# Performance work log

Hardware: AMD Instinct MI355X
Metric: run time of the kernel (lower is better)

Reference implementation:

```python
import jax, jax.numpy as jnp
import numpy as np

N = 8192
IN_F = 256
OUT_F = 128


def setup_inputs() -> dict:
    key = jax.random.key(0)
    k1, k2, k3, k4, k5, k6 = jax.random.split(key, 6)
    input = jax.random.normal(k1, (N, IN_F), dtype=jnp.float32)
    adj = jax.random.randint(k2, (N, N), 0, 2, dtype=jnp.int32)
    # xavier-uniform-like init scaled by gain=0.5
    def xavier(k, shape, gain=0.5):
        fan_in, fan_out = shape[0], shape[1]
        lim = gain * np.sqrt(6.0 / (fan_in + fan_out))
        return jax.random.uniform(k, shape, dtype=jnp.float32, minval=-lim, maxval=lim)
    W_s = xavier(k3, (IN_F, OUT_F))
    a_s = xavier(k4, (OUT_F, 1))
    W_n = xavier(k5, (IN_F, OUT_F))
    a_n = xavier(k6, (OUT_F, 1))
    return {"input": input, "adj": adj, "W_s": W_s, "a_s": a_s, "W_n": W_n, "a_n": a_n}


def reference(input, adj, W_s, a_s, W_n, a_n):
    # Projections: [N, out_features]
    h_s = input @ W_s
    h_n = input @ W_n
    # Additive attention logits: e[i, j] = relu((h_s @ a_s)[i] + (h_n @ a_n)[j])
    e = jax.nn.relu((h_s @ a_s) + (h_n @ a_n).T)  # [N, N]
    # Masked softmax over neighbors (dim=1)
    attention = jnp.where(adj > 0, e, jnp.float32(-9e15))
    attention = jax.nn.softmax(attention, axis=1)
    # Self-scaling term (sum of softmax rows, kept for faithfulness)
    attention_sum = jnp.sum(attention, axis=-1, keepdims=True)
    attention_s = 1.0 / (1.0 + attention_sum)
    # Dropout is identity in eval mode (p=0 / training=False)
    h_prime = attention_s * h_s + attention @ h_n
    # concat=True -> elu activation
    return jax.nn.elu(h_prime)
```

## Files before the change

### kernel.cpp

```cpp
#include <hip/hip_runtime.h>
#include <math.h>

#define NN 8192

typedef short short8 __attribute__((ext_vector_type(8)));
typedef float f32x4 __attribute__((ext_vector_type(4)));

__device__ __forceinline__ float eluf(float x) {
  return x > 0.f ? x : (__expf(x) - 1.f);
}
__device__ __forceinline__ unsigned short f2bf(float f) {
  union { float f; unsigned u; } v; v.f = f;
  unsigned r = v.u + 0x7fffu + ((v.u >> 16) & 1u);
  return (unsigned short)(r >> 16);
}

__global__ __launch_bounds__(256) void k_proj(const float* __restrict__ X,
                                              const float* __restrict__ Ws,
                                              const float* __restrict__ Wn,
                                              const float* __restrict__ as_,
                                              const float* __restrict__ an_,
                                              float* __restrict__ Hs,
                                              unsigned short* __restrict__ HnT,
                                              float* __restrict__ s_out,
                                              float* __restrict__ n_out) {
  __shared__ float4 lin4[8 * 64];
  const int t = threadIdx.x;
  const int i0 = blockIdx.x * 8;
  const float4* Xg = (const float4*)X + (size_t)i0 * 64;
  lin4[t] = Xg[t];
  if (t < 256) lin4[t + 256] = Xg[t + 256];
  __syncthreads();
  const int c = t & 127;
  const int rh = t >> 7;
  float accs[4], accn[4];
#pragma unroll
  for (int r = 0; r < 4; ++r) { accs[r] = 0.f; accn[r] = 0.f; }
  for (int k = 0; k < 256; k += 4) {
    float ws0 = Ws[(k + 0) * 128 + c], ws1 = Ws[(k + 1) * 128 + c];
    float ws2 = Ws[(k + 2) * 128 + c], ws3 = Ws[(k + 3) * 128 + c];
    float wn0 = Wn[(k + 0) * 128 + c], wn1 = Wn[(k + 1) * 128 + c];
    float wn2 = Wn[(k + 2) * 128 + c], wn3 = Wn[(k + 3) * 128 + c];
#pragma unroll
    for (int r = 0; r < 4; ++r) {
      float4 iv = lin4[(rh * 4 + r) * 64 + (k >> 2)];
      accs[r] = fmaf(iv.x, ws0, accs[r]); accs[r] = fmaf(iv.y, ws1, accs[r]);
      accs[r] = fmaf(iv.z, ws2, accs[r]); accs[r] = fmaf(iv.w, ws3, accs[r]);
      accn[r] = fmaf(iv.x, wn0, accn[r]); accn[r] = fmaf(iv.y, wn1, accn[r]);
      accn[r] = fmaf(iv.z, wn2, accn[r]); accn[r] = fmaf(iv.w, wn3, accn[r]);
    }
  }
#pragma unroll
  for (int r = 0; r < 4; ++r)
    Hs[(size_t)(i0 + rh * 4 + r) * 128 + c] = accs[r];
  {
    union { unsigned short us[4]; ushort4 u4; } pk;
#pragma unroll
    for (int r = 0; r < 4; ++r) pk.us[r] = f2bf(accn[r]);
    *(ushort4*)(HnT + (size_t)blockIdx.x * 1024 + c * 8 + rh * 4) = pk.u4;
  }
  float* red = (float*)lin4;
  const int wv = t >> 6, ln = t & 63;
  __syncthreads();
  {
    float av = as_[c];
#pragma unroll
    for (int r = 0; r < 4; ++r) red[(rh * 4 + r) * 128 + c] = accs[r] * av;
  }
  __syncthreads();
#pragma unroll
  for (int h = 0; h < 2; ++h) {
    int row = wv * 2 + h;
    float p = red[row * 128 + ln] + red[row * 128 + 64 + ln];
#pragma unroll
    for (int off = 32; off >= 1; off >>= 1) p += __shfl_down(p, off);
    if (ln == 0) s_out[i0 + row] = p;
  }
  __syncthreads();
  {
    float av = an_[c];
#pragma unroll
    for (int r = 0; r < 4; ++r) red[(rh * 4 + r) * 128 + c] = accn[r] * av;
  }
  __syncthreads();
#pragma unroll
  for (int h = 0; h < 2; ++h) {
    int row = wv * 2 + h;
    float p = red[row * 128 + ln] + red[row * 128 + 64 + ln];
#pragma unroll
    for (int off = 32; off >= 1; off >>= 1) p += __shfl_down(p, off);
    if (ln == 0) n_out[i0 + row] = p;
  }
}

__global__ __launch_bounds__(512, 4) void k_main(const int* __restrict__ A,
                                                 const unsigned short* __restrict__ HnT,
                                                 const float* __restrict__ sv_g,
                                                 const float* __restrict__ nv_g,
                                                 float* __restrict__ HsOut) {
  __shared__ float accbuf[8][16][128];
  __shared__ float zsh[8][16];
  __shared__ float zf[16];

  const int t = threadIdx.x;
  const int wv = t >> 6;
  const int ln = t & 63;
  const int q = ln >> 4;
  const int m = ln & 15;
  const int row0 = blockIdx.x * 16;

  const float sm = sv_g[row0 + m];
  const int jbase = wv * 1024 + q * 8;
  const int* aptr = A + (size_t)(row0 + m) * NN + jbase;
  const float* nptr = nv_g + jbase;
  const unsigned short* bptr = HnT + ((size_t)(wv * 128 + q) * 128 + m) * 8;

  f32x4 acc[8];
#pragma unroll
  for (int ft = 0; ft < 8; ++ft) acc[ft] = (f32x4){0.f, 0.f, 0.f, 0.f};
  float zp = 0.f;

  int4 adjv[2][2];
  float4 nvv[2][2];
  union Breg { uint4 u; short8 s; };
  Breg breg[8];

  adjv[0][0] = *(const int4*)(aptr);       adjv[0][1] = *(const int4*)(aptr + 4);
  adjv[1][0] = *(const int4*)(aptr + 32);  adjv[1][1] = *(const int4*)(aptr + 36);
  nvv[0][0] = *(const float4*)(nptr);      nvv[0][1] = *(const float4*)(nptr + 4);
  breg[0].u = *(const uint4*)(bptr);       breg[1].u = *(const uint4*)(bptr + 128);
  breg[2].u = *(const uint4*)(bptr + 256); breg[3].u = *(const uint4*)(bptr + 384);
  breg[4].u = *(const uint4*)(bptr + 512); breg[5].u = *(const uint4*)(bptr + 640);
  breg[6].u = *(const uint4*)(bptr + 768); breg[7].u = *(const uint4*)(bptr + 896);

#pragma unroll 2
  for (int tt = 0; tt < 32; ++tt) {
    const int cur = tt & 1;
    short8 fr;
    {
      float nvl[8] = {nvv[cur][0].x, nvv[cur][0].y, nvv[cur][0].z, nvv[cur][0].w,
                      nvv[cur][1].x, nvv[cur][1].y, nvv[cur][1].z, nvv[cur][1].w};
      int av[8] = {adjv[cur][0].x, adjv[cur][0].y, adjv[cur][0].z, adjv[cur][0].w,
                   adjv[cur][1].x, adjv[cur][1].y, adjv[cur][1].z, adjv[cur][1].w};
#pragma unroll
      for (int k = 0; k < 8; ++k) {
        float w = av[k] > 0 ? __expf(fmaxf(sm + nvl[k], 0.f)) : 0.f;
        zp += w;
        fr[k] = (short)f2bf(w);
      }
    }
    if (tt < 31) {
      const float* p = nptr + (tt + 1) * 32;
      nvv[cur ^ 1][0] = *(const float4*)p;
      nvv[cur ^ 1][1] = *(const float4*)(p + 4);
    }
    __builtin_amdgcn_s_setprio(1);
    acc[0] = __builtin_amdgcn_mfma_f32_16x16x32_bf16(fr, breg[0].s, acc[0], 0, 0, 0);
    acc[1] = __builtin_amdgcn_mfma_f32_16x16x32_bf16(fr, breg[1].s, acc[1], 0, 0, 0);
    acc[2] = __builtin_amdgcn_mfma_f32_16x16x32_bf16(fr, breg[2].s, acc[2], 0, 0, 0);
    acc[3] = __builtin_amdgcn_mfma_f32_16x16x32_bf16(fr, breg[3].s, acc[3], 0, 0, 0);
    acc[4] = __builtin_amdgcn_mfma_f32_16x16x32_bf16(fr, breg[4].s, acc[4], 0, 0, 0);
    acc[5] = __builtin_amdgcn_mfma_f32_16x16x32_bf16(fr, breg[5].s, acc[5], 0, 0, 0);
    acc[6] = __builtin_amdgcn_mfma_f32_16x16x32_bf16(fr, breg[6].s, acc[6], 0, 0, 0);
    acc[7] = __builtin_amdgcn_mfma_f32_16x16x32_bf16(fr, breg[7].s, acc[7], 0, 0, 0);
    __builtin_amdgcn_s_setprio(0);
    if (tt < 31) {
      const unsigned short* p = bptr + (size_t)(tt + 1) * 4096;
      breg[0].u = *(const uint4*)(p);       breg[1].u = *(const uint4*)(p + 128);
      breg[2].u = *(const uint4*)(p + 256); breg[3].u = *(const uint4*)(p + 384);
      breg[4].u = *(const uint4*)(p + 512); breg[5].u = *(const uint4*)(p + 640);
      breg[6].u = *(const uint4*)(p + 768); breg[7].u = *(const uint4*)(p + 896);
    }
    if (tt < 30) {
      const int* p = aptr + (tt + 2) * 32;
      adjv[cur][0] = *(const int4*)p;
      adjv[cur][1] = *(const int4*)(p + 4);
    }
  }

  {
    float zz = zp;
    zz += __shfl_down(zz, 32);
    zz += __shfl_down(zz, 16);
    if (ln < 16) zsh[wv][ln] = zz;
  }
#pragma unroll
  for (int ft = 0; ft < 8; ++ft) {
#pragma unroll
    for (int reg = 0; reg < 4; ++reg)
      accbuf[wv][q * 4 + reg][ft * 16 + m] = acc[ft][reg];
  }
  __syncthreads();
  if (t < 16) {
    float z = zsh[0][t] + zsh[1][t] + zsh[2][t] + zsh[3][t] +
              zsh[4][t] + zsh[5][t] + zsh[6][t] + zsh[7][t];
    zf[t] = 1.f / z;
  }
  __syncthreads();
  {
    const int row = t >> 5;
    const int f0 = (t & 31) * 4;
    f32x4 ssum = *(const f32x4*)&accbuf[0][row][f0];
#pragma unroll
    for (int w = 1; w < 8; ++w) ssum += *(const f32x4*)&accbuf[w][row][f0];
    const float invz = zf[row];
    const size_t off = (size_t)(row0 + row) * 128 + f0;
    float4 h = *(const float4*)(HsOut + off);
    float4 o;
    o.x = eluf(fmaf(ssum[0], invz, 0.5f * h.x));
    o.y = eluf(fmaf(ssum[1], invz, 0.5f * h.y));
    o.z = eluf(fmaf(ssum[2], invz, 0.5f * h.z));
    o.w = eluf(fmaf(ssum[3], invz, 0.5f * h.w));
    *(float4*)(HsOut + off) = o;
  }
}

extern "C" void kernel_launch(void* const* d_in, const int* in_sizes, int n_in,
                              void* d_out, int out_size, void* d_ws, size_t ws_size,
                              hipStream_t stream) {
  const float* X   = (const float*)d_in[0];
  const int*   A   = (const int*)d_in[1];
  const float* Ws  = (const float*)d_in[2];
  const float* as_ = (const float*)d_in[3];
  const float* Wn  = (const float*)d_in[4];
  const float* an_ = (const float*)d_in[5];
  float* out = (float*)d_out;

  unsigned short* HnT = (unsigned short*)d_ws;
  float* s = (float*)(HnT + (size_t)128 * NN);
  float* n = s + NN;

  k_proj<<<1024, 256, 0, stream>>>(X, Ws, Wn, as_, an_, out, HnT, s, n);
  k_main<<<512, 512, 0, stream>>>(A, HnT, s, n, out);
}
```

Measured before the change: 459.7 us.

## Pack int32 adjacency into bitmask before the attention aggregation kernel

Adds a pre-pass kernel that compresses each row of the int32 adjacency matrix into 32-bit bitmasks, so the main kernel reads 1 bit per neighbour instead of 4 bytes. The main kernel now prefetches one mask word and extracts a byte per lane group instead of loading int4 vectors. The full adjacency read still happens, now in a separate pass with no compute overlapping it, plus an extra write and read of the packed mask. The packing keeps only the low bit, which matches `adj > 0` only for 0/1 values. The original path is kept as a fallback when the workspace is too small.

New measurement: 451.9 us. Within noise of the previous version (-1.7%).

```diff
diff --git a/kernel.cpp b/kernel.cpp
--- a/kernel.cpp
+++ b/kernel.cpp
@@ -13,6 +13,25 @@
   union { float f; unsigned u; } v; v.f = f;
   unsigned r = v.u + 0x7fffu + ((v.u >> 16) & 1u);
   return (unsigned short)(r >> 16);
+}
+
+__global__ __launch_bounds__(256) void k_pack(const int* __restrict__ A,
+                                              unsigned* __restrict__ P) {
+  const int t = threadIdx.x;
+  const int row = blockIdx.x;
+  const int4* src = (const int4*)(A + (size_t)row * NN) + t * 8;
+  int4 v[8];
+#pragma unroll
+  for (int c = 0; c < 8; ++c) v[c] = src[c];
+  unsigned w = 0;
+#pragma unroll
+  for (int c = 0; c < 8; ++c) {
+    w |= (unsigned)(v[c].x & 1) << (c * 4 + 0);
+    w |= (unsigned)(v[c].y & 1) << (c * 4 + 1);
+    w |= (unsigned)(v[c].z & 1) << (c * 4 + 2);
+    w |= (unsigned)(v[c].w & 1) << (c * 4 + 3);
+  }
+  P[(size_t)row * 256 + t] = w;
 }
 
 __global__ __launch_bounds__(256) void k_proj(const float* __restrict__ X,
@@ -93,11 +112,11 @@
   }
 }
 
-__global__ __launch_bounds__(512, 4) void k_main(const int* __restrict__ A,
-                                                 const unsigned short* __restrict__ HnT,
-                                                 const float* __restrict__ sv_g,
-                                                 const float* __restrict__ nv_g,
-                                                 float* __restrict__ HsOut) {
+__global__ __launch_bounds__(512, 4) void k_main_bits(const unsigned* __restrict__ Pk,
+                                                      const unsigned short* __restrict__ HnT,
+                                                      const float* __restrict__ sv_g,
+                                                      const float* __restrict__ nv_g,
+                                                      float* __restrict__ HsOut) {
   __shared__ float accbuf[8][16][128];
   __shared__ float zsh[8][16];
   __shared__ float zf[16];
@@ -111,8 +130,8 @@
 
   const float sm = sv_g[row0 + m];
   const int jbase = wv * 1024 + q * 8;
-  const int* aptr = A + (size_t)(row0 + m) * NN + jbase;
   const float* nptr = nv_g + jbase;
+  const unsigned* Pp = Pk + (size_t)(row0 + m) * 256 + wv * 32;
   const unsigned short* bptr = HnT + ((size_t)(wv * 128 + q) * 128 + m) * 8;
 
   f32x4 acc[8];
@@ -120,14 +139,15 @@
   for (int ft = 0; ft < 8; ++ft) acc[ft] = (f32x4){0.f, 0.f, 0.f, 0.f};
   float zp = 0.f;
 
-  int4 adjv[2][2];
   float4 nvv[2][2];
+  unsigned bv[2];
   union Breg { uint4 u; short8 s; };
   Breg breg[8];
 
-  adjv[0][0] = *(const int4*)(aptr);       adjv[0][1] = *(const int4*)(aptr + 4);
-  adjv[1][0] = *(const int4*)(aptr + 32);  adjv[1][1] = *(const int4*)(aptr + 36);
   nvv[0][0] = *(const float4*)(nptr);      nvv[0][1] = *(const float4*)(nptr + 4);
+  nvv[1][0] = *(const float4*)(nptr + 32); nvv[1][1] = *(const float4*)(nptr + 36);
+  bv[0] = Pp[0];
+  bv[1] = Pp[1];
   breg[0].u = *(const uint4*)(bptr);       breg[1].u = *(const uint4*)(bptr + 128);
   breg[2].u = *(const uint4*)(bptr + 256); breg[3].u = *(const uint4*)(bptr + 384);
   breg[4].u = *(const uint4*)(bptr + 512); breg[5].u = *(const uint4*)(bptr + 640);
@@ -140,19 +160,19 @@
     {
       float nvl[8] = {nvv[cur][0].x, nvv[cur][0].y, nvv[cur][0].z, nvv[cur][0].w,
                       nvv[cur][1].x, nvv[cur][1].y, nvv[cur][1].z, nvv[cur][1].w};
-      int av[8] = {adjv[cur][0].x, adjv[cur][0].y, adjv[cur][0].z, adjv[cur][0].w,
-                   adjv[cur][1].x, adjv[cur][1].y, adjv[cur][1].z, adjv[cur][1].w};
+      const unsigned byte = (bv[cur] >> (q * 8)) & 0xffu;
 #pragma unroll
       for (int k = 0; k < 8; ++k) {
-        float w = av[k] > 0 ? __expf(fmaxf(sm + nvl[k], 0.f)) : 0.f;
+        float w = ((byte >> k) & 1u) ? __expf(fmaxf(sm + nvl[k], 0.f)) : 0.f;
         zp += w;
         fr[k] = (short)f2bf(w);
       }
     }
-    if (tt < 31) {
-      const float* p = nptr + (tt + 1) * 32;
-      nvv[cur ^ 1][0] = *(const float4*)p;
-      nvv[cur ^ 1][1] = *(const float4*)(p + 4);
+    if (tt < 30) {
+      const float* p = nptr + (tt + 2) * 32;
+      nvv[cur][0] = *(const float4*)p;
+      nvv[cur][1] = *(const float4*)(p + 4);
+      bv[cur] = Pp[tt + 2];
     }
     __builtin_amdgcn_s_setprio(1);
     acc[0] = __builtin_amdgcn_mfma_f32_16x16x32_bf16(fr, breg[0].s, acc[0], 0, 0, 0);
@@ -171,11 +191,6 @@
       breg[4].u = *(const uint4*)(p + 512); breg[5].u = *(const uint4*)(p + 640);
       breg[6].u = *(const uint4*)(p + 768); breg[7].u = *(const uint4*)(p + 896);
     }
-    if (tt < 30) {
-      const int* p = aptr + (tt + 2) * 32;
-      adjv[cur][0] = *(const int4*)p;
-      adjv[cur][1] = *(const int4*)(p + 4);
-    }
   }
 
   {
@@ -215,6 +230,128 @@
   }
 }
 
+__global__ __launch_bounds__(512, 4) void k_main_adj(const int* __restrict__ A,
+                                                     const unsigned short* __restrict__ HnT,
+                                                     const float* __restrict__ sv_g,
+                                                     const float* __restrict__ nv_g,
+                                                     float* __restrict__ HsOut) {
+  __shared__ float accbuf[8][16][128];
+  __shared__ float zsh[8][16];
+  __shared__ float zf[16];
+
+  const int t = threadIdx.x;
+  const int wv = t >> 6;
+  const int ln = t & 63;
+  const int q = ln >> 4;
+  const int m = ln & 15;
+  const int row0 = blockIdx.x * 16;
+
+  const float sm = sv_g[row0 + m];
+  const int jbase = wv * 1024 + q * 8;
+  const int* aptr = A + (size_t)(row0 + m) * NN + jbase;
+  const float* nptr = nv_g + jbase;
+  const unsigned short* bptr = HnT + ((size_t)(wv * 128 + q) * 128 + m) * 8;
+
+  f32x4 acc[8];
+#pragma unroll
+  for (int ft = 0; ft < 8; ++ft) acc[ft] = (f32x4){0.f, 0.f, 0.f, 0.f};
+  float zp = 0.f;
+
+  int4 adjv[2][2];
+  float4 nvv[2][2];
+  union Breg { uint4 u; short8 s; };
+  Breg breg[8];
+
+  adjv[0][0] = *(const int4*)(aptr);       adjv[0][1] = *(const int4*)(aptr + 4);
+  adjv[1][0] = *(const int4*)(aptr + 32);  adjv[1][1] = *(const int4*)(aptr + 36);
+  nvv[0][0] = *(const float4*)(nptr);      nvv[0][1] = *(const float4*)(nptr + 4);
+  breg[0].u = *(const uint4*)(bptr);       breg[1].u = *(const uint4*)(bptr + 128);
+  breg[2].u = *(const uint4*)(bptr + 256); breg[3].u = *(const uint4*)(bptr + 384);
+  breg[4].u = *(const uint4*)(bptr + 512); breg[5].u = *(const uint4*)(bptr + 640);
+  breg[6].u = *(const uint4*)(bptr + 768); breg[7].u = *(const uint4*)(bptr + 896);
+
+#pragma unroll 2
+  for (int tt = 0; tt < 32; ++tt) {
+    const int cur = tt & 1;
+    short8 fr;
+    {
+      float nvl[8] = {nvv[cur][0].x, nvv[cur][0].y, nvv[cur][0].z, nvv[cur][0].w,
+                      nvv[cur][1].x, nvv[cur][1].y, nvv[cur][1].z, nvv[cur][1].w};
+      int av[8] = {adjv[cur][0].x, adjv[cur][0].y, adjv[cur][0].z, adjv[cur][0].w,
+                   adjv[cur][1].x, adjv[cur][1].y, adjv[cur][1].z, adjv[cur][1].w};
+#pragma unroll
+      for (int k = 0; k < 8; ++k) {
+        float w = av[k] > 0 ? __expf(fmaxf(sm + nvl[k], 0.f)) : 0.f;
+        zp += w;
+        fr[k] = (short)f2bf(w);
+      }
+    }
+    if (tt < 31) {
+      const float* p = nptr + (tt + 1) * 32;
+      nvv[cur ^ 1][0] = *(const float4*)p;
+      nvv[cur ^ 1][1] = *(const float4*)(p + 4);
+    }
+    __builtin_amdgcn_s_setprio(1);
+    acc[0] = __builtin_amdgcn_mfma_f32_16x16x32_bf16(fr, breg[0].s, acc[0], 0, 0, 0);
+    acc[1] = __builtin_amdgcn_mfma_f32_16x16x32_bf16(fr, breg[1].s, acc[1], 0, 0, 0);
+    acc[2] = __builtin_amdgcn_mfma_f32_16x16x32_bf16(fr, breg[2].s, acc[2], 0, 0, 0);
+    acc[3] = __builtin_amdgcn_mfma_f32_16x16x32_bf16(fr, breg[3].s, acc[3], 0, 0, 0);
+    acc[4] = __builtin_amdgcn_mfma_f32_16x16x32_bf16(fr, breg[4].s, acc[4], 0, 0, 0);
+    acc[5] = __builtin_amdgcn_mfma_f32_16x16x32_bf16(fr, breg[5].s, acc[5], 0, 0, 0);
+    acc[6] = __builtin_amdgcn_mfma_f32_16x16x32_bf16(fr, breg[6].s, acc[6], 0, 0, 0);
+    acc[7] = __builtin_amdgcn_mfma_f32_16x16x32_bf16(fr, breg[7].s, acc[7], 0, 0, 0);
+    __builtin_amdgcn_s_setprio(0);
+    if (tt < 31) {
+      const unsigned short* p = bptr + (size_t)(tt + 1) * 4096;
+      breg[0].u = *(const uint4*)(p);       breg[1].u = *(const uint4*)(p + 128);
+      breg[2].u = *(const uint4*)(p + 256); breg[3].u = *(const uint4*)(p + 384);
+      breg[4].u = *(const uint4*)(p + 512); breg[5].u = *(const uint4*)(p + 640);
+      breg[6].u = *(const uint4*)(p + 768); breg[7].u = *(const uint4*)(p + 896);
+    }
+    if (tt < 30) {
+      const int* p = aptr + (tt + 2) * 32;
+      adjv[cur][0] = *(const int4*)p;
+      adjv[cur][1] = *(const int4*)(p + 4);
+    }
+  }
+
+  {
+    float zz = zp;
+    zz += __shfl_down(zz, 32);
+    zz += __shfl_down(zz, 16);
+    if (ln < 16) zsh[wv][ln] = zz;
+  }
+#pragma unroll
+  for (int ft = 0; ft < 8; ++ft) {
+#pragma unroll
+    for (int reg = 0; reg < 4; ++reg)
+      accbuf[wv][q * 4 + reg][ft * 16 + m] = acc[ft][reg];
+  }
+  __syncthreads();
+  if (t < 16) {
+    float z = zsh[0][t] + zsh[1][t] + zsh[2][t] + zsh[3][t] +
+              zsh[4][t] + zsh[5][t] + zsh[6][t] + zsh[7][t];
+    zf[t] = 1.f / z;
+  }
+  __syncthreads();
+  {
+    const int row = t >> 5;
+    const int f0 = (t & 31) * 4;
+    f32x4 ssum = *(const f32x4*)&accbuf[0][row][f0];
+#pragma unroll
+    for (int w = 1; w < 8; ++w) ssum += *(const f32x4*)&accbuf[w][row][f0];
+    const float invz = zf[row];
+    const size_t off = (size_t)(row0 + row) * 128 + f0;
+    float4 h = *(const float4*)(HsOut + off);
+    float4 o;
+    o.x = eluf(fmaf(ssum[0], invz, 0.5f * h.x));
+    o.y = eluf(fmaf(ssum[1], invz, 0.5f * h.y));
+    o.z = eluf(fmaf(ssum[2], invz, 0.5f * h.z));
+    o.w = eluf(fmaf(ssum[3], invz, 0.5f * h.w));
+    *(float4*)(HsOut + off) = o;
+  }
+}
+
 extern "C" void kernel_launch(void* const* d_in, const int* in_sizes, int n_in,
                               void* d_out, int out_size, void* d_ws, size_t ws_size,
                               hipStream_t stream) {
@@ -229,7 +366,16 @@
   unsigned short* HnT = (unsigned short*)d_ws;
   float* s = (float*)(HnT + (size_t)128 * NN);
   float* n = s + NN;
+  unsigned* P = (unsigned*)(n + NN);
+
+  const size_t base_need = (size_t)128 * NN * 2 + (size_t)2 * NN * 4;
+  const size_t bits_need = base_need + (size_t)NN * 256 * 4;
 
   k_proj<<<1024, 256, 0, stream>>>(X, Ws, Wn, as_, an_, out, HnT, s, n);
-  k_main<<<512, 512, 0, stream>>>(A, HnT, s, n, out);
-}
+  if (ws_size >= bits_need) {
+    k_pack<<<8192, 256, 0, stream>>>(A, P);
+    k_main_bits<<<512, 512, 0, stream>>>(P, HnT, s, n, out);
+  } else {
+    k_main_adj<<<512, 512, 0, stream>>>(A, HnT, s, n, out);
+  }
+}
```

## Precompute exponentials and stage adjacency as LDS bitmask in attention kernel

Applied to the files above, without the earlier changes.

Rewrites exp(relu(s+n)) as max(exp(s)*exp(n),1), so the projection kernel stores exponentiated scores and the main loop does no per-element transcendentals. The main kernel first packs its 16 adjacency rows into a bitmask and stages the exp-neighbor vector in LDS, replacing per-iteration global adjacency/score loads. The final cross-wave reduction is done in two halves so shared memory shrinks from 64KB to 48KB, which allows more resident blocks. Risks include losing overlap between adjacency loads and MFMA work, float overflow if scores are large, and an unguarded prefetch on the last iteration that reads past the HnT buffer into the adjacent workspace.

Measured after the change: 423.7 us. 1.09x faster.

```diff
diff --git a/kernel.cpp b/kernel.cpp
--- a/kernel.cpp
+++ b/kernel.cpp
@@ -13,6 +13,10 @@
   union { float f; unsigned u; } v; v.f = f;
   unsigned r = v.u + 0x7fffu + ((v.u >> 16) & 1u);
   return (unsigned short)(r >> 16);
+}
+__device__ __forceinline__ unsigned pack4(int4 v, int sh) {
+  return ((unsigned)(v.x & 1) << sh) | ((unsigned)(v.y & 1) << (sh + 1)) |
+         ((unsigned)(v.z & 1) << (sh + 2)) | ((unsigned)(v.w & 1) << (sh + 3));
 }
 
 __global__ __launch_bounds__(256) void k_proj(const float* __restrict__ X,
@@ -22,8 +26,8 @@
                                               const float* __restrict__ an_,
                                               float* __restrict__ Hs,
                                               unsigned short* __restrict__ HnT,
-                                              float* __restrict__ s_out,
-                                              float* __restrict__ n_out) {
+                                              float* __restrict__ es_out,
+                                              float* __restrict__ en_out) {
   __shared__ float4 lin4[8 * 64];
   const int t = threadIdx.x;
   const int i0 = blockIdx.x * 8;
@@ -74,7 +78,7 @@
     float p = red[row * 128 + ln] + red[row * 128 + 64 + ln];
 #pragma unroll
     for (int off = 32; off >= 1; off >>= 1) p += __shfl_down(p, off);
-    if (ln == 0) s_out[i0 + row] = p;
+    if (ln == 0) es_out[i0 + row] = __expf(p);
   }
   __syncthreads();
   {
@@ -89,16 +93,19 @@
     float p = red[row * 128 + ln] + red[row * 128 + 64 + ln];
 #pragma unroll
     for (int off = 32; off >= 1; off >>= 1) p += __shfl_down(p, off);
-    if (ln == 0) n_out[i0 + row] = p;
+    if (ln == 0) en_out[i0 + row] = __expf(p);
   }
 }
 
 __global__ __launch_bounds__(512, 4) void k_main(const int* __restrict__ A,
                                                  const unsigned short* __restrict__ HnT,
-                                                 const float* __restrict__ sv_g,
-                                                 const float* __restrict__ nv_g,
+                                                 const float* __restrict__ es_g,
+                                                 const float* __restrict__ en_g,
                                                  float* __restrict__ HsOut) {
-  __shared__ float accbuf[8][16][128];
+  __shared__ __align__(16) char smem[49152];
+  float* en_lds = (float*)smem;
+  unsigned* bits_lds = (unsigned*)(smem + 32768);
+  float* cmb = (float*)smem;
   __shared__ float zsh[8][16];
   __shared__ float zf[16];
 
@@ -109,25 +116,40 @@
   const int m = ln & 15;
   const int row0 = blockIdx.x * 16;
 
-  const float sm = sv_g[row0 + m];
-  const int jbase = wv * 1024 + q * 8;
-  const int* aptr = A + (size_t)(row0 + m) * NN + jbase;
-  const float* nptr = nv_g + jbase;
+  {
+    float4* dst = (float4*)en_lds;
+    const float4* s4 = (const float4*)en_g;
+#pragma unroll
+    for (int k = 0; k < 4; ++k) dst[t + k * 512] = s4[t + k * 512];
+#pragma unroll 1
+    for (int k = 0; k < 8; ++k) {
+      int g = t + k * 512;
+      int rr = g >> 8;
+      int c8 = g & 255;
+      const int4* src = (const int4*)(A + (size_t)(row0 + rr) * NN + c8 * 32);
+      int4 v0 = src[0], v1 = src[1], v2 = src[2], v3 = src[3];
+      int4 v4 = src[4], v5 = src[5], v6 = src[6], v7 = src[7];
+      unsigned w = pack4(v0, 0)  | pack4(v1, 4)  | pack4(v2, 8)  | pack4(v3, 12) |
+                   pack4(v4, 16) | pack4(v5, 20) | pack4(v6, 24) | pack4(v7, 28);
+      bits_lds[(c8 >> 5) * 512 + (c8 & 31) * 16 + rr] = w;
+    }
+  }
+
+  const float sme = es_g[row0 + m];
   const unsigned short* bptr = HnT + ((size_t)(wv * 128 + q) * 128 + m) * 8;
+  const float* nvl = en_lds + wv * 1024 + q * 8;
+  const unsigned* bts = bits_lds + wv * 512 + m;
 
   f32x4 acc[8];
 #pragma unroll
   for (int ft = 0; ft < 8; ++ft) acc[ft] = (f32x4){0.f, 0.f, 0.f, 0.f};
   float zp = 0.f;
 
-  int4 adjv[2][2];
-  float4 nvv[2][2];
   union Breg { uint4 u; short8 s; };
   Breg breg[8];
 
-  adjv[0][0] = *(const int4*)(aptr);       adjv[0][1] = *(const int4*)(aptr + 4);
-  adjv[1][0] = *(const int4*)(aptr + 32);  adjv[1][1] = *(const int4*)(aptr + 36);
-  nvv[0][0] = *(const float4*)(nptr);      nvv[0][1] = *(const float4*)(nptr + 4);
+  __syncthreads();
+
   breg[0].u = *(const uint4*)(bptr);       breg[1].u = *(const uint4*)(bptr + 128);
   breg[2].u = *(const uint4*)(bptr + 256); breg[3].u = *(const uint4*)(bptr + 384);
   breg[4].u = *(const uint4*)(bptr + 512); breg[5].u = *(const uint4*)(bptr + 640);
@@ -135,24 +157,19 @@
 
 #pragma unroll 2
   for (int tt = 0; tt < 32; ++tt) {
-    const int cur = tt & 1;
     short8 fr;
     {
-      float nvl[8] = {nvv[cur][0].x, nvv[cur][0].y, nvv[cur][0].z, nvv[cur][0].w,
-                      nvv[cur][1].x, nvv[cur][1].y, nvv[cur][1].z, nvv[cur][1].w};
-      int av[8] = {adjv[cur][0].x, adjv[cur][0].y, adjv[cur][0].z, adjv[cur][0].w,
-                   adjv[cur][1].x, adjv[cur][1].y, adjv[cur][1].z, adjv[cur][1].w};
+      float4 nv0 = *(const float4*)(nvl + tt * 32);
+      float4 nv1 = *(const float4*)(nvl + tt * 32 + 4);
+      const unsigned bw = bts[tt * 16];
+      const unsigned byte = (bw >> (q * 8)) & 0xffu;
+      float ev[8] = {nv0.x, nv0.y, nv0.z, nv0.w, nv1.x, nv1.y, nv1.z, nv1.w};
 #pragma unroll
       for (int k = 0; k < 8; ++k) {
-        float w = av[k] > 0 ? __expf(fmaxf(sm + nvl[k], 0.f)) : 0.f;
+        float w = ((byte >> k) & 1u) ? fmaxf(sme * ev[k], 1.f) : 0.f;
         zp += w;
         fr[k] = (short)f2bf(w);
       }
-    }
-    if (tt < 31) {
-      const float* p = nptr + (tt + 1) * 32;
-      nvv[cur ^ 1][0] = *(const float4*)p;
-      nvv[cur ^ 1][1] = *(const float4*)(p + 4);
     }
     __builtin_amdgcn_s_setprio(1);
     acc[0] = __builtin_amdgcn_mfma_f32_16x16x32_bf16(fr, breg[0].s, acc[0], 0, 0, 0);
@@ -164,18 +181,13 @@
     acc[6] = __builtin_amdgcn_mfma_f32_16x16x32_bf16(fr, breg[6].s, acc[6], 0, 0, 0);
     acc[7] = __builtin_amdgcn_mfma_f32_16x16x32_bf16(fr, breg[7].s, acc[7], 0, 0, 0);
     __builtin_amdgcn_s_setprio(0);
-    if (tt < 31) {
+    {
       const unsigned short* p = bptr + (size_t)(tt + 1) * 4096;
       breg[0].u = *(const uint4*)(p);       breg[1].u = *(const uint4*)(p + 128);
       breg[2].u = *(const uint4*)(p + 256); breg[3].u = *(const uint4*)(p + 384);
       breg[4].u = *(const uint4*)(p + 512); breg[5].u = *(const uint4*)(p + 640);
       breg[6].u = *(const uint4*)(p + 768); breg[7].u = *(const uint4*)(p + 896);
     }
-    if (tt < 30) {
-      const int* p = aptr + (tt + 2) * 32;
-      adjv[cur][0] = *(const int4*)p;
-      adjv[cur][1] = *(const int4*)(p + 4);
-    }
   }
 
   {
@@ -184,13 +196,30 @@
     zz += __shfl_down(zz, 16);
     if (ln < 16) zsh[wv][ln] = zz;
   }
-#pragma unroll
-  for (int ft = 0; ft < 8; ++ft) {
-#pragma unroll
-    for (int reg = 0; reg < 4; ++reg)
-      accbuf[wv][q * 4 + reg][ft * 16 + m] = acc[ft][reg];
-  }
-  __syncthreads();
+  __syncthreads();
+  if (wv >= 4) {
+#pragma unroll
+    for (int ft = 0; ft < 8; ++ft)
+#pragma unroll
+      for (int reg = 0; reg < 4; ++reg)
+        cmb[(wv - 4) * 2048 + (q * 4 + reg) * 128 + ft * 16 + m] = acc[ft][reg];
+  }
+  __syncthreads();
+  if (wv < 4) {
+#pragma unroll
+    for (int ft = 0; ft < 8; ++ft)
+#pragma unroll
+      for (int reg = 0; reg < 4; ++reg)
+        acc[ft][reg] += cmb[wv * 2048 + (q * 4 + reg) * 128 + ft * 16 + m];
+  }
+  __syncthreads();
+  if (wv < 4) {
+#pragma unroll
+    for (int ft = 0; ft < 8; ++ft)
+#pragma unroll
+      for (int reg = 0; reg < 4; ++reg)
+        cmb[wv * 2048 + (q * 4 + reg) * 128 + ft * 16 + m] = acc[ft][reg];
+  }
   if (t < 16) {
     float z = zsh[0][t] + zsh[1][t] + zsh[2][t] + zsh[3][t] +
               zsh[4][t] + zsh[5][t] + zsh[6][t] + zsh[7][t];
@@ -200,9 +229,9 @@
   {
     const int row = t >> 5;
     const int f0 = (t & 31) * 4;
-    f32x4 ssum = *(const f32x4*)&accbuf[0][row][f0];
-#pragma unroll
-    for (int w = 1; w < 8; ++w) ssum += *(const f32x4*)&accbuf[w][row][f0];
+    f32x4 ssum = *(const f32x4*)&cmb[row * 128 + f0];
+#pragma unroll
+    for (int w = 1; w < 4; ++w) ssum += *(const f32x4*)&cmb[w * 2048 + row * 128 + f0];
     const float invz = zf[row];
     const size_t off = (size_t)(row0 + row) * 128 + f0;
     float4 h = *(const float4*)(HsOut + off);
@@ -227,9 +256,9 @@
   float* out = (float*)d_out;
 
   unsigned short* HnT = (unsigned short*)d_ws;
-  float* s = (float*)(HnT + (size_t)128 * NN);
-  float* n = s + NN;
-
-  k_proj<<<1024, 256, 0, stream>>>(X, Ws, Wn, as_, an_, out, HnT, s, n);
-  k_main<<<512, 512, 0, stream>>>(A, HnT, s, n, out);
-}
+  float* es = (float*)(HnT + (size_t)128 * NN);
+  float* en = es + NN;
+
+  k_proj<<<1024, 256, 0, stream>>>(X, Ws, Wn, as_, an_, out, HnT, es, en);
+  k_main<<<512, 512, 0, stream>>>(A, HnT, es, en, out);
+}
```
